# Performance work log

Hardware: AMD Instinct MI355X
Metric: run time of the kernel (lower is better)

Reference implementation:

```python
import jax, jax.numpy as jnp
import numpy as np

O, NI, F, D, NN, M = 2048, 16, 4, 128, 8, 8  # outfits, item slots, factors, dim, neighbors, valid slots
D2 = D // 2

def lrelu(x):
    return jax.nn.leaky_relu(x, 0.01)

def mlp2(x, W1, b1, W2, b2):
    # Linear -> LeakyReLU -> Linear -> LeakyReLU (Dropout is identity at inference)
    return lrelu(lrelu(x @ W1 + b1) @ W2 + b2)

def setup_inputs():
    ks = jax.random.split(jax.random.key(0), 16)
    s = 0.05
    pos = jnp.arange(NI)[None, :]
    outfit_items = jnp.where(pos < M, jax.random.randint(ks[0], (O, NI), 0, NI), -1)
    items_neighbor = jax.random.randint(ks[1], (O, NI, NN), -1, NI)
    items_feature = jax.random.normal(ks[2], (O, NI, D), dtype=jnp.float32)
    items_factors = jnp.zeros((O, NI, F, D), dtype=jnp.float32)
    p = {
        'cf_W1': jax.random.normal(ks[3], (F, D, D2)) * s,
        'cf_b1': jnp.zeros((F, D2)),
        'cf_W2': jax.random.normal(ks[4], (F, D2, D)) * s,
        'cf_b2': jnp.zeros((F, D)),
        'f2f_W1': jax.random.normal(ks[5], (D, D)) * s, 'f2f_b1': jnp.zeros((D,)),
        'f2f_W2': jax.random.normal(ks[6], (D, D)) * s, 'f2f_b2': jnp.zeros((D,)),
        'f2i_W1': jax.random.normal(ks[7], (D, D)) * s, 'f2i_b1': jnp.zeros((D,)),
        'f2i_W2': jax.random.normal(ks[8], (D, D)) * s, 'f2i_b2': jnp.zeros((D,)),
        'i2i_W1': jax.random.normal(ks[9], (D, D)) * s, 'i2i_b1': jnp.zeros((D,)),
        'i2i_W2': jax.random.normal(ks[10], (D, D)) * s, 'i2i_b2': jnp.zeros((D,)),
        'o2s_W': jax.random.normal(ks[11], (D, 1)) * s, 'o2s_b': jnp.zeros((1,)),
    }
    return dict(outfit_items=outfit_items, items_feature=items_feature,
                items_neighbor=items_neighbor, items_factors=items_factors, **p)

def _forward(outfit_items, items_feature, items_neighbor, items_factors,
             cf_W1, cf_b1, cf_W2, cf_b2, f2f_W1, f2f_b1, f2f_W2, f2f_b2,
             f2i_W1, f2i_b1, f2i_W2, f2i_b2, i2i_W1, i2i_b1, i2i_W2, i2i_b2,
             o2s_W, o2s_b):
    del items_factors  # creat_factors overwrites every entry in the original
    # --- creat_factors: per-factor 2-layer MLP on every item feature -> [O,NI,F,D]
    h = lrelu(jnp.einsum('oid,fde->oife', items_feature, cf_W1) + cf_b1)
    fac = lrelu(jnp.einsum('oife,fed->oifd', h, cf_W2) + cf_b2)

    # --- inter_factors: sequential over outfit slots; later slots read updated factors
    def outfit_fac(fac_o, oi_o, nbr_o):
        def step(f, i):
            valid = i != -1
            ic = jnp.maximum(i, 0)
            cand = jnp.concatenate([oi_o, nbr_o[ic]])                # [NI+NN]
            cm = (cand != -1) & (cand != i) & valid
            t = f[ic]                                                # [F,D] snapshot
            msg = mlp2(t[None] * f[jnp.maximum(cand, 0)],
                       f2f_W1, f2f_b1, f2f_W2, f2f_b2)               # [NI+NN,F,D]
            add = jnp.sum(jnp.where(cm[:, None, None], msg, 0.0), axis=0)
            return f.at[ic].add(jnp.where(valid, add, 0.0)), None
        f, _ = jax.lax.scan(step, fac_o, oi_o)
        return f
    fac = jax.vmap(outfit_fac)(fac, outfit_items, items_neighbor)

    # --- infer_items: feature[i] += sum_j f2i(fac[i,j]) for outfit members
    g = mlp2(fac, f2i_W1, f2i_b1, f2i_W2, f2i_b2).sum(axis=2)        # [O,NI,D]
    ic = jnp.maximum(outfit_items, 0)
    w = (outfit_items != -1).astype(g.dtype)                          # [O,NI]
    gsel = jnp.take_along_axis(g, ic[..., None], axis=1)
    scat = jax.vmap(lambda gs, idx, ww: jnp.zeros((NI, D), gs.dtype).at[idx].add(ww[:, None] * gs))
    feat = items_feature + scat(gsel, ic, w)

    # --- inter_items: sequential; current value detached (.data in original)
    def outfit_feat(fo_init, oi_o):
        jc = jnp.maximum(oi_o, 0)
        def step(fo, i):
            valid = i != -1
            ic_ = jnp.maximum(i, 0)
            t = jax.lax.stop_gradient(fo[ic_])
            msgs = mlp2(fo[jc], i2i_W1, i2i_b1, i2i_W2, i2i_b2)      # [NI,D]
            m = ((oi_o != -1) & (oi_o != i)).astype(fo.dtype)
            new = t + jnp.sum(m[:, None] * msgs, axis=0)
            return jnp.where(valid, fo.at[ic_].set(new), fo), None
        fo, _ = jax.lax.scan(step, fo_init, oi_o)
        return fo
    feat = jax.vmap(outfit_feat)(feat, outfit_items)

    # --- infer_outfit + score
    fsel = jnp.take_along_axis(feat, ic[..., None], axis=1)
    outfits = jnp.sum(w[..., None] * fsel, axis=1)                    # [O,D]
    scores = jax.nn.sigmoid(outfits @ o2s_W + o2s_b)[:, 0]            # [O]

    # --- com_loss: ||F F^T - I||_F^2 over valid slots (positional mask), / n_outfits
    G = jnp.einsum('oifd,oigd->oifg', fac, fac) - jnp.eye(F, dtype=fac.dtype)
    com = jnp.sum(w * jnp.sum(G * G, axis=(-1, -2))) / O
    return scores, jnp.reshape(com, (1,))

def reference(outfit_items, items_feature, items_neighbor, items_factors,
              cf_W1, cf_b1, cf_W2, cf_b2, f2f_W1, f2f_b1, f2f_W2, f2f_b2,
              f2i_W1, f2i_b1, f2i_W2, f2i_b2, i2i_W1, i2i_b1, i2i_W2, i2i_b2,
              o2s_W, o2s_b):
    return _forward(outfit_items, items_feature, items_neighbor, items_factors,
                    cf_W1, cf_b1, cf_W2, cf_b2, f2f_W1, f2f_b1, f2f_W2, f2f_b2,
                    f2i_W1, f2i_b1, f2i_W2, f2i_b2, i2i_W1, i2i_b1, i2i_W2, i2i_b2,
                    o2s_W, o2s_b)
```

## Files before the change

### kernel.cpp

```cpp
#include <hip/hip_runtime.h>
#include <hip/hip_bf16.h>
#include <math.h>


typedef __attribute__((ext_vector_type(8))) short short8;
typedef __attribute__((ext_vector_type(4))) float f32x4;

#define MFMA16(a, b, c) __builtin_amdgcn_mfma_f32_16x16x32_bf16(a, b, c, 0, 0, 0)

__device__ __forceinline__ float lrelu(float x) { return fmaxf(x, 0.01f * x); }

__device__ __forceinline__ ushort f2bf(float f) {
  unsigned u = __builtin_bit_cast(unsigned, f);
  u += 0x7fffu + ((u >> 16) & 1u);
  return (ushort)(u >> 16);
}
__device__ __forceinline__ float bflo(unsigned u) {
  return __builtin_bit_cast(float, u << 16);
}
__device__ __forceinline__ unsigned pk2(float a, float b) {
  float2 t; t.x = a; t.y = b;
  __hip_bfloat162 h = __float22bfloat162_rn(t);
  unsigned u;
  __builtin_memcpy(&u, &h, 4);
  return u;
}


__global__ __launch_bounds__(256) void prep_weights(
    const float* __restrict__ cfW1, const float* __restrict__ cfW2,
    const float* __restrict__ f2fW1, const float* __restrict__ f2fW2,
    const float* __restrict__ f2iW1, const float* __restrict__ f2iW2,
    const float* __restrict__ i2iW1, const float* __restrict__ i2iW2,
    ushort* __restrict__ ws, float* __restrict__ out) {
  const int idx = (int)(blockIdx.x * 256 + threadIdx.x);
  if (idx == 0) out[2048] = 0.0f;
  float v;
  if (idx < 32768) {
    int f = idx >> 13, r = idx & 8191, n = r >> 7, k = r & 127;
    v = cfW1[f * 8192 + k * 64 + n];
  } else if (idx < 65536) {
    int t = idx - 32768;
    int f = t >> 13, r = t & 8191, n = r >> 6, k = r & 63;
    v = cfW2[f * 8192 + k * 128 + n];
  } else {
    int t = idx - 65536;
    int seg = t >> 14, r = t & 16383, n = r >> 7, k = r & 127;
    const float* W = (seg == 0) ? f2fW1 : (seg == 1) ? f2fW2 :
                     (seg == 2) ? f2iW1 : (seg == 3) ? f2iW2 :
                     (seg == 4) ? i2iW1 : i2iW2;
    v = W[k * 128 + n];
  }
  ws[idx] = f2bf(v);
}

__global__ __launch_bounds__(512, 2) void mfgn_kernel(
    const int* __restrict__ outfit_items,
    const float* __restrict__ items_feature,
    const int* __restrict__ items_neighbor,
    const float* __restrict__ cfb1, const float* __restrict__ cfb2,
    const float* __restrict__ f2fb1, const float* __restrict__ f2fb2,
    const float* __restrict__ f2ib1, const float* __restrict__ f2ib2,
    const float* __restrict__ i2ib1, const float* __restrict__ i2ib2,
    const float* __restrict__ o2sW, const float* __restrict__ o2sb,
    const ushort* __restrict__ wsW,
    float* __restrict__ out)
{
  __shared__ float facL[16 * 528];
  __shared__ ushort prodS[8192] __attribute__((aligned(16)));
  __shared__ ushort hidS[8192] __attribute__((aligned(16)));
  __shared__ ushort featB[2048] __attribute__((aligned(16)));
  __shared__ float redE[8];
  __shared__ int oiL[16];
  __shared__ int clAll[256];
  __shared__ int ncAll[16];
  __shared__ int vslL[16];
  __shared__ int refcntL[16];
  __shared__ int nvsL;

  const int o = blockIdx.x;
  const int tid = (int)threadIdx.x;
  const int lane = tid & 63;
  const int wid = tid >> 6;
  const int n16 = lane & 15;
  const int q = lane >> 4;
  const int kb = q * 8;
  const int col = wid * 16 + n16;
  const int lx = lane * 8;
  const int fS = lane & 3, ciS = lane >> 2;
  const int kc0 = wid * 16;
  const int q0 = (wid & 1) * 2;
  const int sWA = ((wid >> 1) * 4 + (lane >> 4)) * 512 + (lane & 15) * 8;
  const int hwB = (wid >> 1) * 2048 + ((wid & 1) * 2 + (q >> 1)) * 128 + n16 * 8 + (q & 1) * 4;
  const int fbCol = (col >> 5) * 512 + ((col >> 3) & 3) * 128 + (col & 7);

  if (tid < 16) oiL[tid] = outfit_items[o * 16 + tid];
  {
    const int n = tid >> 5, d0 = (tid & 31) * 4;
    float4 v = *(const float4*)(items_feature + o * 2048 + tid * 4);
    uint2 pk; pk.x = pk2(v.x, v.y); pk.y = pk2(v.z, v.w);
    *(uint2*)(featB + (d0 >> 5) * 512 + (((d0 >> 3) & 3) * 16 + n) * 8 + (d0 & 7)) = pk;
  }
  if (tid == 0) {
    int cnt = 0;
    for (int s = 0; s < 16; ++s) refcntL[s] = 0;
    for (int s = 0; s < 16; ++s) {
      int v = oiL[s];
      if (v != -1) { vslL[cnt++] = s; refcntL[v]++; }
    }
    nvsL = cnt;
  }
  for (int s = wid; s < 16; s += 8) {
    const int iv = outfit_items[o * 16 + s];
    if (iv == -1) { if (lane == 0) ncAll[s] = 0; continue; }
    int cand = -1;
    if (lane < 24) cand = (lane < 16) ? outfit_items[o * 16 + lane]
                                      : items_neighbor[o * 128 + iv * 8 + (lane - 16)];
    bool ok = (lane < 24) && (cand != -1) && (cand != iv);
    unsigned long long bm = __ballot(ok);
    if (ok) clAll[s * 16 + __popcll(bm & ((1ull << lane) - 1ull))] = cand;
    if (lane == 0) ncAll[s] = (int)__popcll(bm);
  }
  __syncthreads();
  const int nvs = nvsL;

  {
    const int f = wid & 3, half = wid >> 2;
    short8 wA[2][4];
#pragma unroll
    for (int etl = 0; etl < 2; ++etl)
#pragma unroll
      for (int kt = 0; kt < 4; ++kt)
        wA[etl][kt] = *(const short8*)(wsW + (f * 64 + (half * 2 + etl) * 16 + n16) * 128
                                       + kt * 32 + kb);
    f32x4 acc[2];
#pragma unroll
    for (int etl = 0; etl < 2; ++etl)
      acc[etl] = *(const f32x4*)(cfb1 + f * 64 + (half * 2 + etl) * 16 + q * 4);
    for (int kt = 0; kt < 4; ++kt) {
      short8 x = *(const short8*)(featB + kt * 512 + lx);
      acc[0] = MFMA16(wA[0][kt], x, acc[0]);
      acc[1] = MFMA16(wA[1][kt], x, acc[1]);
    }
#pragma unroll
    for (int etl = 0; etl < 2; ++etl) {
      float h0 = lrelu(acc[etl][0]), h1 = lrelu(acc[etl][1]);
      float h2 = lrelu(acc[etl][2]), h3 = lrelu(acc[etl][3]);
      uint2 pk; pk.x = pk2(h0, h1); pk.y = pk2(h2, h3);
      *(uint2*)(hidS + half * 2048 + f * 512 + (etl * 2 + (q >> 1)) * 128
                + n16 * 8 + (q & 1) * 4) = pk;
    }
    __syncthreads();
    short8 wB[4][2];
#pragma unroll
    for (int ctl = 0; ctl < 4; ++ctl)
#pragma unroll
      for (int kt = 0; kt < 2; ++kt)
        wB[ctl][kt] = *(const short8*)(wsW + 32768 + (f * 128 + half * 64 + ctl * 16 + n16) * 64
                                       + kt * 32 + kb);
    f32x4 acc2[4];
#pragma unroll
    for (int ctl = 0; ctl < 4; ++ctl) {
      float b2 = cfb2[f * 128 + half * 64 + ctl * 16 + n16];
      acc2[ctl] = (f32x4){b2, b2, b2, b2};
    }
    for (int kt = 0; kt < 2; ++kt) {
      short8 h = *(const short8*)(hidS + (kt * 4 + f) * 512 + lx);
#pragma unroll
      for (int ctl = 0; ctl < 4; ++ctl) acc2[ctl] = MFMA16(h, wB[ctl][kt], acc2[ctl]);
    }
#pragma unroll
    for (int ctl = 0; ctl < 4; ++ctl) {
      int c = half * 64 + ctl * 16 + n16;
#pragma unroll
      for (int r = 0; r < 4; ++r)
        facL[(q * 4 + r) * 528 + f * 132 + c] = lrelu(acc2[ctl][r]);
    }
    __syncthreads();
  }

  {
    short8 w1f[4], w2f[4];
#pragma unroll
    for (int kt = 0; kt < 4; ++kt) {
      w1f[kt] = *(const short8*)(wsW + 65536 + col * 128 + kt * 32 + kb);
      w2f[kt] = *(const short8*)(wsW + 81920 + col * 128 + kt * 32 + kb);
    }
    const f32x4 b1q = *(const f32x4*)(f2fb1 + wid * 16 + q * 4);
    const float b2v = f2fb2[col];

    auto stageB = [&](int s, int iv_, int nc_) {
      if (ciS < nc_) {
        const int cit = clAll[s * 16 + ciS];
        const float* tp = facL + iv_ * 528 + fS * 132 + kc0;
        const float* cp = facL + cit * 528 + fS * 132 + kc0;
#pragma unroll
        for (int g = 0; g < 2; ++g) {
          float4 a0 = *(const float4*)(tp + g * 8), a1 = *(const float4*)(tp + g * 8 + 4);
          float4 c0 = *(const float4*)(cp + g * 8), c1 = *(const float4*)(cp + g * 8 + 4);
          uint4 u4;
          u4.x = pk2(a0.x * c0.x, a0.y * c0.y); u4.y = pk2(a0.z * c0.z, a0.w * c0.w);
          u4.z = pk2(a1.x * c1.x, a1.y * c1.y); u4.w = pk2(a1.z * c1.z, a1.w * c1.w);
          *(uint4*)(prodS + sWA + (q0 + g) * 128) = u4;
        }
      }
    };
    auto stageC = [&]() {
      const float* sp = facL + ciS * 528 + fS * 132 + kc0;
#pragma unroll
      for (int g = 0; g < 2; ++g) {
        float4 a0 = *(const float4*)(sp + g * 8), a1 = *(const float4*)(sp + g * 8 + 4);
        uint4 u4;
        u4.x = pk2(a0.x, a0.y); u4.y = pk2(a0.z, a0.w);
        u4.z = pk2(a1.x, a1.y); u4.w = pk2(a1.z, a1.w);
        *(uint4*)(prodS + sWA + (q0 + g) * 128) = u4;
      }
    };

    if (nvs > 0) { const int s0 = vslL[0]; stageB(s0, oiL[s0], ncAll[s0]); }
    __syncthreads();

    for (int u = 0; u < nvs; ++u) {
      const int s = vslL[u];
      const int iv = oiL[s];
      const int nc = ncAll[s];
      f32x4 acc[4];
#pragma unroll
      for (int mt = 0; mt < 4; ++mt) acc[mt] = b1q;
      for (int kt = 0; kt < 4; ++kt)
#pragma unroll
        for (int mt = 0; mt < 4; ++mt) {
          short8 x = *(const short8*)(prodS + (kt * 4 + mt) * 512 + lx);
          acc[mt] = MFMA16(w1f[kt], x, acc[mt]);
        }
#pragma unroll
      for (int mt = 0; mt < 4; ++mt) {
        float h0 = lrelu(acc[mt][0]), h1 = lrelu(acc[mt][1]);
        float h2 = lrelu(acc[mt][2]), h3 = lrelu(acc[mt][3]);
        uint2 pk; pk.x = pk2(h0, h1); pk.y = pk2(h2, h3);
        *(uint2*)(hidS + hwB + mt * 512) = pk;
      }
      __syncthreads();
      f32x4 acc2[4];
#pragma unroll
      for (int mt = 0; mt < 4; ++mt) acc2[mt] = (f32x4){b2v, b2v, b2v, b2v};
      for (int kt = 0; kt < 4; ++kt)
#pragma unroll
        for (int mt = 0; mt < 4; ++mt) {
          short8 h = *(const short8*)(hidS + (kt * 4 + mt) * 512 + lx);
          acc2[mt] = MFMA16(h, w2f[kt], acc2[mt]);
        }
      float part[4] = {0.f, 0.f, 0.f, 0.f};
#pragma unroll
      for (int mt = 0; mt < 4; ++mt) {
        bool act = (mt * 4 + q) < nc;
        if (act) {
#pragma unroll
          for (int r = 0; r < 4; ++r) part[r] += lrelu(acc2[mt][r]);
        }
      }
#pragma unroll
      for (int r = 0; r < 4; ++r) {
        float v = part[r];
        v += __shfl_xor(v, 16);
        v += __shfl_xor(v, 32);
        part[r] = v;
      }
      if (q == 0) {
#pragma unroll
        for (int r = 0; r < 4; ++r)
          facL[iv * 528 + r * 132 + col] += part[r];
      }
      if (u + 1 < nvs) {
        const int s2 = vslL[u + 1];
        stageB(s2, oiL[s2], ncAll[s2]);
      } else {
        stageC();
      }
      __syncthreads();
    }
    if (nvs == 0) { stageC(); __syncthreads(); }
  }

  {
    short8 w1f[4], w2f[4];
#pragma unroll
    for (int kt = 0; kt < 4; ++kt) {
      w1f[kt] = *(const short8*)(wsW + 98304 + col * 128 + kt * 32 + kb);
      w2f[kt] = *(const short8*)(wsW + 114688 + col * 128 + kt * 32 + kb);
    }
    const f32x4 b1q = *(const f32x4*)(f2ib1 + wid * 16 + q * 4);
    const float b2v = f2ib2[col];
    f32x4 acc[4];
#pragma unroll
    for (int mt = 0; mt < 4; ++mt) acc[mt] = b1q;
    for (int kt = 0; kt < 4; ++kt)
#pragma unroll
      for (int mt = 0; mt < 4; ++mt) {
        short8 x = *(const short8*)(prodS + (kt * 4 + mt) * 512 + lx);
        acc[mt] = MFMA16(w1f[kt], x, acc[mt]);
      }
#pragma unroll
    for (int mt = 0; mt < 4; ++mt) {
      float h0 = lrelu(acc[mt][0]), h1 = lrelu(acc[mt][1]);
      float h2 = lrelu(acc[mt][2]), h3 = lrelu(acc[mt][3]);
      uint2 pk; pk.x = pk2(h0, h1); pk.y = pk2(h2, h3);
      *(uint2*)(hidS + hwB + mt * 512) = pk;
    }
    __syncthreads();
    f32x4 acc2[4];
#pragma unroll
    for (int mt = 0; mt < 4; ++mt) acc2[mt] = (f32x4){b2v, b2v, b2v, b2v};
    for (int kt = 0; kt < 4; ++kt)
#pragma unroll
      for (int mt = 0; mt < 4; ++mt) {
        short8 h = *(const short8*)(hidS + (kt * 4 + mt) * 512 + lx);
        acc2[mt] = MFMA16(h, w2f[kt], acc2[mt]);
      }
#pragma unroll
    for (int mt = 0; mt < 4; ++mt) {
      int item = mt * 4 + q;
      float g = 0.f;
#pragma unroll
      for (int r = 0; r < 4; ++r) g += lrelu(acc2[mt][r]);
      int a = fbCol + item * 8;
      featB[a] = f2bf(bflo((unsigned)featB[a]) + (float)refcntL[item] * g);
    }
    __syncthreads();
  }

  {
    short8 w1f[4], w2f[4];
#pragma unroll
    for (int kt = 0; kt < 4; ++kt) {
      w1f[kt] = *(const short8*)(wsW + 131072 + col * 128 + kt * 32 + kb);
      w2f[kt] = *(const short8*)(wsW + 147456 + col * 128 + kt * 32 + kb);
    }
    const f32x4 b1q = *(const f32x4*)(i2ib1 + wid * 16 + q * 4);
    const float b2v = i2ib2[col];
    short8 xc[4];
#pragma unroll
    for (int kt = 0; kt < 4; ++kt)
      xc[kt] = *(const short8*)(featB + kt * 512 + lx);

    for (int u = 0; u < nvs; ++u) {
      const int iv = oiL[vslL[u]];
      f32x4 acc = b1q;
      for (int kt = 0; kt < 4; ++kt) acc = MFMA16(w1f[kt], xc[kt], acc);
      {
        float h0 = lrelu(acc[0]), h1 = lrelu(acc[1]);
        float h2 = lrelu(acc[2]), h3 = lrelu(acc[3]);
        uint2 pk; pk.x = pk2(h0, h1); pk.y = pk2(h2, h3);
        *(uint2*)(hidS + hwB) = pk;
      }
      __syncthreads();
      f32x4 acc2 = (f32x4){b2v, b2v, b2v, b2v};
      for (int kt = 0; kt < 4; ++kt) {
        short8 h = *(const short8*)(hidS + kt * 2048 + lx);
        acc2 = MFMA16(h, w2f[kt], acc2);
      }
      float part = 0.f;
#pragma unroll
      for (int r = 0; r < 4; ++r) {
        int item = q * 4 + r;
        float w = (item == iv) ? 0.0f : (float)refcntL[item];
        part += w * lrelu(acc2[r]);
      }
      part += __shfl_xor(part, 16);
      part += __shfl_xor(part, 32);
      if (q == 0) {
        int a = fbCol + iv * 8;
        featB[a] = f2bf(bflo((unsigned)featB[a]) + part);
      }
      __syncthreads();
      if (n16 == iv) {
#pragma unroll
        for (int kt = 0; kt < 4; ++kt)
          xc[kt] = *(const short8*)(featB + kt * 512 + lx);
      }
    }
  }

  if (tid < 128) {
    const int eb = (tid >> 5) * 512 + ((tid >> 3) & 3) * 128 + (tid & 7);
    float sum = 0.0f;
    for (int u = 0; u < nvs; ++u) {
      int it = oiL[vslL[u]];
      sum += bflo((unsigned)featB[eb + it * 8]);
    }
    float v = sum * o2sW[tid];
#pragma unroll
    for (int off = 1; off < 64; off <<= 1) v += __shfl_xor(v, off);
    if (lane == 0) redE[wid] = v;
  }
  __syncthreads();
  if (tid == 0) {
    float t = redE[0] + redE[1] + o2sb[0];
    out[o] = 1.0f / (1.0f + expf(-t));
  }

  {
    const int n = tid >> 5, f = (tid >> 3) & 3, g = (tid >> 1) & 3, h = tid & 1;
    float dot = 0.0f;
    if (f <= g) {
      const float* pa = facL + n * 528 + f * 132 + h * 64;
      const float* pb = facL + n * 528 + g * 132 + h * 64;
      for (int i = 0; i < 16; ++i) {
        float4 a = *(const float4*)(pa + i * 4);
        float4 b = *(const float4*)(pb + i * 4);
        dot += a.x * b.x + a.y * b.y + a.z * b.z + a.w * b.w;
      }
    }
    dot += __shfl_xor(dot, 1);
    float v = dot - ((f == g) ? 1.0f : 0.0f);
    float wgt = (f == g) ? 1.0f : 2.0f;
    float sq = (h == 0 && f <= g && oiL[n] != -1) ? wgt * v * v : 0.0f;
#pragma unroll
    for (int off = 1; off < 64; off <<= 1) sq += __shfl_xor(sq, off);
    __syncthreads();
    if (lane == 0) redE[wid] = sq;
    __syncthreads();
    if (tid == 0) {
      float tot = 0.f;
#pragma unroll
      for (int w = 0; w < 8; ++w) tot += redE[w];
      atomicAdd(out + 2048, tot * (1.0f / 2048.0f));
    }
  }
}

extern "C" void kernel_launch(void* const* d_in, const int* in_sizes, int n_in,
                              void* d_out, int out_size, void* d_ws, size_t ws_size,
                              hipStream_t stream) {
  float* out = (float*)d_out;
  ushort* ws = (ushort*)d_ws;
  hipLaunchKernelGGL(prep_weights, dim3(640), dim3(256), 0, stream,
                     (const float*)d_in[4], (const float*)d_in[6],
                     (const float*)d_in[8], (const float*)d_in[10],
                     (const float*)d_in[12], (const float*)d_in[14],
                     (const float*)d_in[16], (const float*)d_in[18],
                     ws, out);
  hipLaunchKernelGGL(mfgn_kernel, dim3(2048), dim3(512), 0, stream,
                     (const int*)d_in[0],
                     (const float*)d_in[1],
                     (const int*)d_in[2],
                     (const float*)d_in[5], (const float*)d_in[7],
                     (const float*)d_in[9], (const float*)d_in[11],
                     (const float*)d_in[13], (const float*)d_in[15],
                     (const float*)d_in[17], (const float*)d_in[19],
                     (const float*)d_in[20], (const float*)d_in[21],
                     (const ushort*)ws,
                     out);
}
```

Measured before the change: 320.9 us.

## Overlap next-slot staging with MLP and interleave Gram loss into i2i loop

In the f2f loop, the product staging for the next slot now runs right after the second MFMA stage instead of after the facL update. Rows that depend on the item just updated are recomputed afterwards, which moves most staging work off the critical path before the barrier. The com_loss Gram dot products are spread across the i2i loop barriers in small steps, and their reduction is merged into the final score write. This removes a separate tail phase and two barriers, but adds redundant staging work and a correctness risk if the dependency check misses a case.

```diff
diff --git a/kernel.cpp b/kernel.cpp
--- a/kernel.cpp
+++ b/kernel.cpp
@@ -71,6 +71,7 @@
   __shared__ ushort hidS[8192] __attribute__((aligned(16)));
   __shared__ ushort featB[2048] __attribute__((aligned(16)));
   __shared__ float redE[8];
+  __shared__ float redF[8];
   __shared__ int oiL[16];
   __shared__ int clAll[256];
   __shared__ int ncAll[16];
@@ -189,23 +190,20 @@
     const f32x4 b1q = *(const f32x4*)(f2fb1 + wid * 16 + q * 4);
     const float b2v = f2fb2[col];
 
-    auto stageB = [&](int s, int iv_, int nc_) {
-      if (ciS < nc_) {
-        const int cit = clAll[s * 16 + ciS];
-        const float* tp = facL + iv_ * 528 + fS * 132 + kc0;
-        const float* cp = facL + cit * 528 + fS * 132 + kc0;
-#pragma unroll
-        for (int g = 0; g < 2; ++g) {
-          float4 a0 = *(const float4*)(tp + g * 8), a1 = *(const float4*)(tp + g * 8 + 4);
-          float4 c0 = *(const float4*)(cp + g * 8), c1 = *(const float4*)(cp + g * 8 + 4);
-          uint4 u4;
-          u4.x = pk2(a0.x * c0.x, a0.y * c0.y); u4.y = pk2(a0.z * c0.z, a0.w * c0.w);
-          u4.z = pk2(a1.x * c1.x, a1.y * c1.y); u4.w = pk2(a1.z * c1.z, a1.w * c1.w);
-          *(uint4*)(prodS + sWA + (q0 + g) * 128) = u4;
-        }
+    auto stageRow = [&](int ivR, int citR) {
+      const float* tp = facL + ivR * 528 + fS * 132 + kc0;
+      const float* cp = facL + citR * 528 + fS * 132 + kc0;
+#pragma unroll
+      for (int g = 0; g < 2; ++g) {
+        float4 a0 = *(const float4*)(tp + g * 8), a1 = *(const float4*)(tp + g * 8 + 4);
+        float4 c0 = *(const float4*)(cp + g * 8), c1 = *(const float4*)(cp + g * 8 + 4);
+        uint4 u4;
+        u4.x = pk2(a0.x * c0.x, a0.y * c0.y); u4.y = pk2(a0.z * c0.z, a0.w * c0.w);
+        u4.z = pk2(a1.x * c1.x, a1.y * c1.y); u4.w = pk2(a1.z * c1.z, a1.w * c1.w);
+        *(uint4*)(prodS + sWA + (q0 + g) * 128) = u4;
       }
     };
-    auto stageC = [&]() {
+    auto stageCRow = [&]() {
       const float* sp = facL + ciS * 528 + fS * 132 + kc0;
 #pragma unroll
       for (int g = 0; g < 2; ++g) {
@@ -217,7 +215,10 @@
       }
     };
 
-    if (nvs > 0) { const int s0 = vslL[0]; stageB(s0, oiL[s0], ncAll[s0]); }
+    if (nvs > 0) {
+      const int s0 = vslL[0];
+      if (ciS < ncAll[s0]) stageRow(oiL[s0], clAll[s0 * 16 + ciS]);
+    }
     __syncthreads();
 
     for (int u = 0; u < nvs; ++u) {
@@ -250,6 +251,15 @@
           short8 h = *(const short8*)(hidS + (kt * 4 + mt) * 512 + lx);
           acc2[mt] = MFMA16(h, w2f[kt], acc2[mt]);
         }
+      const bool lastu = (u + 1 >= nvs);
+      int iv2 = -1, cit2 = -1;
+      if (!lastu) {
+        const int s2 = vslL[u + 1];
+        iv2 = oiL[s2];
+        if (ciS < ncAll[s2]) { cit2 = clAll[s2 * 16 + ciS]; stageRow(iv2, cit2); }
+      } else {
+        stageCRow();
+      }
       float part[4] = {0.f, 0.f, 0.f, 0.f};
 #pragma unroll
       for (int mt = 0; mt < 4; ++mt) {
@@ -271,15 +281,14 @@
         for (int r = 0; r < 4; ++r)
           facL[iv * 528 + r * 132 + col] += part[r];
       }
-      if (u + 1 < nvs) {
-        const int s2 = vslL[u + 1];
-        stageB(s2, oiL[s2], ncAll[s2]);
+      if (!lastu) {
+        if (cit2 >= 0 && (cit2 == iv || iv2 == iv)) stageRow(iv2, cit2);
       } else {
-        stageC();
+        if (ciS == iv) stageCRow();
       }
       __syncthreads();
     }
-    if (nvs == 0) { stageC(); __syncthreads(); }
+    if (nvs == 0) { stageCRow(); __syncthreads(); }
   }
 
   {
@@ -330,6 +339,20 @@
   }
 
   {
+    const int nF = tid >> 5, fF = (tid >> 3) & 3, gF = (tid >> 1) & 3, hF = tid & 1;
+    const float* paF = facL + nF * 528 + fF * 132 + hF * 64;
+    const float* pbF = facL + nF * 528 + gF * 132 + hF * 64;
+    float dotF = 0.0f;
+    int cF = (fF <= gF) ? 0 : 16;
+    auto fstep = [&]() {
+      if (cF < 16) {
+        float4 a = *(const float4*)(paF + cF * 4);
+        float4 b = *(const float4*)(pbF + cF * 4);
+        dotF += a.x * b.x + a.y * b.y + a.z * b.z + a.w * b.w;
+        ++cF;
+      }
+    };
+
     short8 w1f[4], w2f[4];
 #pragma unroll
     for (int kt = 0; kt < 4; ++kt) {
@@ -353,6 +376,7 @@
         uint2 pk; pk.x = pk2(h0, h1); pk.y = pk2(h2, h3);
         *(uint2*)(hidS + hwB) = pk;
       }
+      fstep();
       __syncthreads();
       f32x4 acc2 = (f32x4){b2v, b2v, b2v, b2v};
       for (int kt = 0; kt < 4; ++kt) {
@@ -372,6 +396,7 @@
         int a = fbCol + iv * 8;
         featB[a] = f2bf(bflo((unsigned)featB[a]) + part);
       }
+      fstep();
       __syncthreads();
       if (n16 == iv) {
 #pragma unroll
@@ -379,7 +404,17 @@
           xc[kt] = *(const short8*)(featB + kt * 512 + lx);
       }
     }
-  }
+
+    for (int t2 = 0; t2 < 16; ++t2) fstep();
+    dotF += __shfl_xor(dotF, 1);
+    float vF = dotF - ((fF == gF) ? 1.0f : 0.0f);
+    float wgtF = (fF == gF) ? 1.0f : 2.0f;
+    float sqF = (hF == 0 && fF <= gF && oiL[nF] != -1) ? wgtF * vF * vF : 0.0f;
+#pragma unroll
+    for (int off = 1; off < 64; off <<= 1) sqF += __shfl_xor(sqF, off);
+    if (lane == 0) redF[wid] = sqF;
+  }
+  __syncthreads();
 
   if (tid < 128) {
     const int eb = (tid >> 5) * 512 + ((tid >> 3) & 3) * 128 + (tid & 7);
@@ -397,35 +432,10 @@
   if (tid == 0) {
     float t = redE[0] + redE[1] + o2sb[0];
     out[o] = 1.0f / (1.0f + expf(-t));
-  }
-
-  {
-    const int n = tid >> 5, f = (tid >> 3) & 3, g = (tid >> 1) & 3, h = tid & 1;
-    float dot = 0.0f;
-    if (f <= g) {
-      const float* pa = facL + n * 528 + f * 132 + h * 64;
-      const float* pb = facL + n * 528 + g * 132 + h * 64;
-      for (int i = 0; i < 16; ++i) {
-        float4 a = *(const float4*)(pa + i * 4);
-        float4 b = *(const float4*)(pb + i * 4);
-        dot += a.x * b.x + a.y * b.y + a.z * b.z + a.w * b.w;
-      }
-    }
-    dot += __shfl_xor(dot, 1);
-    float v = dot - ((f == g) ? 1.0f : 0.0f);
-    float wgt = (f == g) ? 1.0f : 2.0f;
-    float sq = (h == 0 && f <= g && oiL[n] != -1) ? wgt * v * v : 0.0f;
-#pragma unroll
-    for (int off = 1; off < 64; off <<= 1) sq += __shfl_xor(sq, off);
-    __syncthreads();
-    if (lane == 0) redE[wid] = sq;
-    __syncthreads();
-    if (tid == 0) {
-      float tot = 0.f;
-#pragma unroll
-      for (int w = 0; w < 8; ++w) tot += redE[w];
-      atomicAdd(out + 2048, tot * (1.0f / 2048.0f));
-    }
+    float tot = 0.f;
+#pragma unroll
+    for (int w = 0; w < 8; ++w) tot += redF[w];
+    atomicAdd(out + 2048, tot * (1.0f / 2048.0f));
   }
 }
 
```

After: 325.7 us. About the same (+1.5%).

## Switch f2f and f2i MLPs to 32x32x16 MFMA tiles with 2D wave split

Applied to the files above, without the earlier changes.

Replaces the 16x16x32 MFMA formulation of the factor-to-factor and factor-to-item MLPs with 32x32x16 bf16 MFMAs. Waves are arranged as a 2x4 grid over rows and output columns, and the staging layout in shared memory is changed to match. Weights are now reloaded from global memory for each sequential slot step instead of being held in registers across the loop. Per-column reductions in f2f use shared-memory atomicAdd, and an extra barrier is added per iteration. The aim is fewer MFMA issues and less register pressure, at the cost of repeated weight loads, atomics and more synchronisation.

```diff
diff --git a/kernel.cpp b/kernel.cpp
--- a/kernel.cpp
+++ b/kernel.cpp
@@ -5,8 +5,10 @@
 
 typedef __attribute__((ext_vector_type(8))) short short8;
 typedef __attribute__((ext_vector_type(4))) float f32x4;
+typedef __attribute__((ext_vector_type(16))) float f32x16;
 
 #define MFMA16(a, b, c) __builtin_amdgcn_mfma_f32_16x16x32_bf16(a, b, c, 0, 0, 0)
+#define MFMA32(a, b, c) __builtin_amdgcn_mfma_f32_32x32x16_bf16(a, b, c, 0, 0, 0)
 
 __device__ __forceinline__ float lrelu(float x) { return fmaxf(x, 0.01f * x); }
 
@@ -87,10 +89,13 @@
   const int kb = q * 8;
   const int col = wid * 16 + n16;
   const int lx = lane * 8;
+  const int l31 = lane & 31;
+  const int h = lane >> 5;
+  const int rb = wid >> 2;
+  const int cb = wid & 3;
   const int fS = lane & 3, ciS = lane >> 2;
   const int kc0 = wid * 16;
-  const int q0 = (wid & 1) * 2;
-  const int sWA = ((wid >> 1) * 4 + (lane >> 4)) * 512 + (lane & 15) * 8;
+  const int ubase = (wid * 2 + h) * 512;
   const int hwB = (wid >> 1) * 2048 + ((wid & 1) * 2 + (q >> 1)) * 128 + n16 * 8 + (q & 1) * 4;
   const int fbCol = (col >> 5) * 512 + ((col >> 3) & 3) * 128 + (col & 7);
 
@@ -165,9 +170,9 @@
       acc2[ctl] = (f32x4){b2, b2, b2, b2};
     }
     for (int kt = 0; kt < 2; ++kt) {
-      short8 h = *(const short8*)(hidS + (kt * 4 + f) * 512 + lx);
-#pragma unroll
-      for (int ctl = 0; ctl < 4; ++ctl) acc2[ctl] = MFMA16(h, wB[ctl][kt], acc2[ctl]);
+      short8 hh = *(const short8*)(hidS + (kt * 4 + f) * 512 + lx);
+#pragma unroll
+      for (int ctl = 0; ctl < 4; ++ctl) acc2[ctl] = MFMA16(hh, wB[ctl][kt], acc2[ctl]);
     }
 #pragma unroll
     for (int ctl = 0; ctl < 4; ++ctl) {
@@ -180,14 +185,8 @@
   }
 
   {
-    short8 w1f[4], w2f[4];
-#pragma unroll
-    for (int kt = 0; kt < 4; ++kt) {
-      w1f[kt] = *(const short8*)(wsW + 65536 + col * 128 + kt * 32 + kb);
-      w2f[kt] = *(const short8*)(wsW + 81920 + col * 128 + kt * 32 + kb);
-    }
-    const f32x4 b1q = *(const f32x4*)(f2fb1 + wid * 16 + q * 4);
-    const float b2v = f2fb2[col];
+    const int wrow = cb * 32 + l31;
+    const int oc0 = cb * 32 + 4 * h;
 
     auto stageB = [&](int s, int iv_, int nc_) {
       if (ciS < nc_) {
@@ -201,11 +200,11 @@
           uint4 u4;
           u4.x = pk2(a0.x * c0.x, a0.y * c0.y); u4.y = pk2(a0.z * c0.z, a0.w * c0.w);
           u4.z = pk2(a1.x * c1.x, a1.y * c1.y); u4.w = pk2(a1.z * c1.z, a1.w * c1.w);
-          *(uint4*)(prodS + sWA + (q0 + g) * 128) = u4;
+          *(uint4*)(prodS + ubase + (l31 + g * 32) * 8) = u4;
         }
       }
     };
-    auto stageC = [&]() {
+    auto stageCRow = [&]() {
       const float* sp = facL + ciS * 528 + fS * 132 + kc0;
 #pragma unroll
       for (int g = 0; g < 2; ++g) {
@@ -213,7 +212,7 @@
         uint4 u4;
         u4.x = pk2(a0.x, a0.y); u4.y = pk2(a0.z, a0.w);
         u4.z = pk2(a1.x, a1.y); u4.w = pk2(a1.z, a1.w);
-        *(uint4*)(prodS + sWA + (q0 + g) * 128) = u4;
+        *(uint4*)(prodS + ubase + (l31 + g * 32) * 8) = u4;
       }
     };
 
@@ -224,107 +223,159 @@
       const int s = vslL[u];
       const int iv = oiL[s];
       const int nc = ncAll[s];
-      f32x4 acc[4];
-#pragma unroll
-      for (int mt = 0; mt < 4; ++mt) acc[mt] = b1q;
-      for (int kt = 0; kt < 4; ++kt)
-#pragma unroll
-        for (int mt = 0; mt < 4; ++mt) {
-          short8 x = *(const short8*)(prodS + (kt * 4 + mt) * 512 + lx);
-          acc[mt] = MFMA16(w1f[kt], x, acc[mt]);
-        }
-#pragma unroll
-      for (int mt = 0; mt < 4; ++mt) {
-        float h0 = lrelu(acc[mt][0]), h1 = lrelu(acc[mt][1]);
-        float h2 = lrelu(acc[mt][2]), h3 = lrelu(acc[mt][3]);
-        uint2 pk; pk.x = pk2(h0, h1); pk.y = pk2(h2, h3);
-        *(uint2*)(hidS + hwB + mt * 512) = pk;
+      {
+        short8 wf[8];
+#pragma unroll
+        for (int kt = 0; kt < 8; ++kt)
+          wf[kt] = *(const short8*)(wsW + 65536 + wrow * 128 + kt * 16 + h * 8);
+        float4 ba[4];
+#pragma unroll
+        for (int i = 0; i < 4; ++i)
+          ba[i] = *(const float4*)(f2fb1 + cb * 32 + i * 8 + h * 4);
+        f32x16 acc = {0.f,0.f,0.f,0.f, 0.f,0.f,0.f,0.f, 0.f,0.f,0.f,0.f, 0.f,0.f,0.f,0.f};
+        for (int kt = 0; kt < 8; ++kt) {
+          short8 x = *(const short8*)(prodS + (kt * 2 + rb) * 512 + lx);
+          acc = MFMA32(wf[kt], x, acc);
+        }
+#pragma unroll
+        for (int kt2 = 0; kt2 < 2; ++kt2)
+#pragma unroll
+          for (int hb = 0; hb < 2; ++hb) {
+            const int r0 = kt2 * 8 + hb * 4;
+            const float4 bb = ba[kt2 * 2 + hb];
+            float v0 = lrelu(acc[r0 + 0] + bb.x);
+            float v1 = lrelu(acc[r0 + 1] + bb.y);
+            float v2 = lrelu(acc[r0 + 2] + bb.z);
+            float v3 = lrelu(acc[r0 + 3] + bb.w);
+            uint2 pk; pk.x = pk2(v0, v1); pk.y = pk2(v2, v3);
+            *(uint2*)(hidS + ((cb * 2 + kt2) * 2 + rb) * 512 + (l31 | (hb << 5)) * 8 + h * 4) = pk;
+          }
       }
       __syncthreads();
-      f32x4 acc2[4];
-#pragma unroll
-      for (int mt = 0; mt < 4; ++mt) acc2[mt] = (f32x4){b2v, b2v, b2v, b2v};
-      for (int kt = 0; kt < 4; ++kt)
-#pragma unroll
-        for (int mt = 0; mt < 4; ++mt) {
-          short8 h = *(const short8*)(hidS + (kt * 4 + mt) * 512 + lx);
-          acc2[mt] = MFMA16(h, w2f[kt], acc2[mt]);
-        }
-      float part[4] = {0.f, 0.f, 0.f, 0.f};
-#pragma unroll
-      for (int mt = 0; mt < 4; ++mt) {
-        bool act = (mt * 4 + q) < nc;
-        if (act) {
-#pragma unroll
-          for (int r = 0; r < 4; ++r) part[r] += lrelu(acc2[mt][r]);
-        }
-      }
-#pragma unroll
-      for (int r = 0; r < 4; ++r) {
-        float v = part[r];
-        v += __shfl_xor(v, 16);
-        v += __shfl_xor(v, 32);
-        part[r] = v;
-      }
-      if (q == 0) {
-#pragma unroll
-        for (int r = 0; r < 4; ++r)
-          facL[iv * 528 + r * 132 + col] += part[r];
-      }
+      {
+        short8 wf[8];
+#pragma unroll
+        for (int kt = 0; kt < 8; ++kt)
+          wf[kt] = *(const short8*)(wsW + 81920 + wrow * 128 + kt * 16 + h * 8);
+        float4 ba[4];
+#pragma unroll
+        for (int i = 0; i < 4; ++i)
+          ba[i] = *(const float4*)(f2fb2 + cb * 32 + i * 8 + h * 4);
+        f32x16 acc2 = {0.f,0.f,0.f,0.f, 0.f,0.f,0.f,0.f, 0.f,0.f,0.f,0.f, 0.f,0.f,0.f,0.f};
+        for (int kt = 0; kt < 8; ++kt) {
+          short8 hh = *(const short8*)(hidS + (kt * 2 + rb) * 512 + lx);
+          acc2 = MFMA32(wf[kt], hh, acc2);
+        }
+        float b2r[16];
+#pragma unroll
+        for (int i = 0; i < 4; ++i) {
+          b2r[i * 4 + 0] = ba[i].x; b2r[i * 4 + 1] = ba[i].y;
+          b2r[i * 4 + 2] = ba[i].z; b2r[i * 4 + 3] = ba[i].w;
+        }
+        const bool act = (rb * 8 + (l31 >> 2)) < nc;
+        float part[16];
+#pragma unroll
+        for (int r = 0; r < 16; ++r) {
+          float v = lrelu(acc2[r] + b2r[r]);
+          part[r] = act ? v : 0.0f;
+        }
+#pragma unroll
+        for (int r = 0; r < 16; ++r) {
+          float v = part[r];
+          v += __shfl_xor(v, 4);
+          v += __shfl_xor(v, 8);
+          v += __shfl_xor(v, 16);
+          part[r] = v;
+        }
+        if (l31 < 4) {
+#pragma unroll
+          for (int r = 0; r < 16; ++r)
+            atomicAdd(&facL[iv * 528 + l31 * 132 + oc0 + (r & 3) + 8 * (r >> 2)], part[r]);
+        }
+      }
+      __syncthreads();
       if (u + 1 < nvs) {
         const int s2 = vslL[u + 1];
         stageB(s2, oiL[s2], ncAll[s2]);
       } else {
-        stageC();
+        stageCRow();
       }
       __syncthreads();
     }
-    if (nvs == 0) { stageC(); __syncthreads(); }
+    if (nvs == 0) { stageCRow(); __syncthreads(); }
   }
 
   {
-    short8 w1f[4], w2f[4];
-#pragma unroll
-    for (int kt = 0; kt < 4; ++kt) {
-      w1f[kt] = *(const short8*)(wsW + 98304 + col * 128 + kt * 32 + kb);
-      w2f[kt] = *(const short8*)(wsW + 114688 + col * 128 + kt * 32 + kb);
-    }
-    const f32x4 b1q = *(const f32x4*)(f2ib1 + wid * 16 + q * 4);
-    const float b2v = f2ib2[col];
-    f32x4 acc[4];
-#pragma unroll
-    for (int mt = 0; mt < 4; ++mt) acc[mt] = b1q;
-    for (int kt = 0; kt < 4; ++kt)
-#pragma unroll
-      for (int mt = 0; mt < 4; ++mt) {
-        short8 x = *(const short8*)(prodS + (kt * 4 + mt) * 512 + lx);
-        acc[mt] = MFMA16(w1f[kt], x, acc[mt]);
-      }
-#pragma unroll
-    for (int mt = 0; mt < 4; ++mt) {
-      float h0 = lrelu(acc[mt][0]), h1 = lrelu(acc[mt][1]);
-      float h2 = lrelu(acc[mt][2]), h3 = lrelu(acc[mt][3]);
-      uint2 pk; pk.x = pk2(h0, h1); pk.y = pk2(h2, h3);
-      *(uint2*)(hidS + hwB + mt * 512) = pk;
-    }
-    __syncthreads();
-    f32x4 acc2[4];
-#pragma unroll
-    for (int mt = 0; mt < 4; ++mt) acc2[mt] = (f32x4){b2v, b2v, b2v, b2v};
-    for (int kt = 0; kt < 4; ++kt)
-#pragma unroll
-      for (int mt = 0; mt < 4; ++mt) {
-        short8 h = *(const short8*)(hidS + (kt * 4 + mt) * 512 + lx);
-        acc2[mt] = MFMA16(h, w2f[kt], acc2[mt]);
-      }
-#pragma unroll
-    for (int mt = 0; mt < 4; ++mt) {
-      int item = mt * 4 + q;
-      float g = 0.f;
-#pragma unroll
-      for (int r = 0; r < 4; ++r) g += lrelu(acc2[mt][r]);
-      int a = fbCol + item * 8;
-      featB[a] = f2bf(bflo((unsigned)featB[a]) + (float)refcntL[item] * g);
+    const int wrow = cb * 32 + l31;
+    {
+      short8 wf[8];
+#pragma unroll
+      for (int kt = 0; kt < 8; ++kt)
+        wf[kt] = *(const short8*)(wsW + 98304 + wrow * 128 + kt * 16 + h * 8);
+      float4 ba[4];
+#pragma unroll
+      for (int i = 0; i < 4; ++i)
+        ba[i] = *(const float4*)(f2ib1 + cb * 32 + i * 8 + h * 4);
+      f32x16 acc = {0.f,0.f,0.f,0.f, 0.f,0.f,0.f,0.f, 0.f,0.f,0.f,0.f, 0.f,0.f,0.f,0.f};
+      for (int kt = 0; kt < 8; ++kt) {
+        short8 x = *(const short8*)(prodS + (kt * 2 + rb) * 512 + lx);
+        acc = MFMA32(wf[kt], x, acc);
+      }
+#pragma unroll
+      for (int kt2 = 0; kt2 < 2; ++kt2)
+#pragma unroll
+        for (int hb = 0; hb < 2; ++hb) {
+          const int r0 = kt2 * 8 + hb * 4;
+          const float4 bb = ba[kt2 * 2 + hb];
+          float v0 = lrelu(acc[r0 + 0] + bb.x);
+          float v1 = lrelu(acc[r0 + 1] + bb.y);
+          float v2 = lrelu(acc[r0 + 2] + bb.z);
+          float v3 = lrelu(acc[r0 + 3] + bb.w);
+          uint2 pk; pk.x = pk2(v0, v1); pk.y = pk2(v2, v3);
+          *(uint2*)(hidS + ((cb * 2 + kt2) * 2 + rb) * 512 + (l31 | (hb << 5)) * 8 + h * 4) = pk;
+        }
+    }
+    __syncthreads();
+    {
+      short8 wf[8];
+#pragma unroll
+      for (int kt = 0; kt < 8; ++kt)
+        wf[kt] = *(const short8*)(wsW + 114688 + wrow * 128 + kt * 16 + h * 8);
+      float4 ba[4];
+#pragma unroll
+      for (int i = 0; i < 4; ++i)
+        ba[i] = *(const float4*)(f2ib2 + cb * 32 + i * 8 + h * 4);
+      f32x16 acc2 = {0.f,0.f,0.f,0.f, 0.f,0.f,0.f,0.f, 0.f,0.f,0.f,0.f, 0.f,0.f,0.f,0.f};
+      for (int kt = 0; kt < 8; ++kt) {
+        short8 hh = *(const short8*)(hidS + (kt * 2 + rb) * 512 + lx);
+        acc2 = MFMA32(wf[kt], hh, acc2);
+      }
+      float b2r[16];
+#pragma unroll
+      for (int i = 0; i < 4; ++i) {
+        b2r[i * 4 + 0] = ba[i].x; b2r[i * 4 + 1] = ba[i].y;
+        b2r[i * 4 + 2] = ba[i].z; b2r[i * 4 + 3] = ba[i].w;
+      }
+      float gs[16];
+#pragma unroll
+      for (int r = 0; r < 16; ++r) gs[r] = lrelu(acc2[r] + b2r[r]);
+#pragma unroll
+      for (int r = 0; r < 16; ++r) {
+        float v = gs[r];
+        v += __shfl_xor(v, 1);
+        v += __shfl_xor(v, 2);
+        gs[r] = v;
+      }
+      if ((l31 & 3) == 0) {
+        const int item = rb * 8 + (l31 >> 2);
+        const float rc = (float)refcntL[item];
+#pragma unroll
+        for (int r = 0; r < 16; ++r) {
+          const int c = cb * 32 + (r & 3) + 8 * (r >> 2) + 4 * h;
+          const int a = (c >> 5) * 512 + (((c >> 3) & 3) * 16 + item) * 8 + (c & 7);
+          featB[a] = f2bf(bflo((unsigned)featB[a]) + rc * gs[r]);
+        }
+      }
     }
     __syncthreads();
   }
@@ -356,8 +407,8 @@
       __syncthreads();
       f32x4 acc2 = (f32x4){b2v, b2v, b2v, b2v};
       for (int kt = 0; kt < 4; ++kt) {
-        short8 h = *(const short8*)(hidS + kt * 2048 + lx);
-        acc2 = MFMA16(h, w2f[kt], acc2);
+        short8 hh = *(const short8*)(hidS + kt * 2048 + lx);
+        acc2 = MFMA16(hh, w2f[kt], acc2);
       }
       float part = 0.f;
 #pragma unroll
@@ -400,11 +451,11 @@
   }
 
   {
-    const int n = tid >> 5, f = (tid >> 3) & 3, g = (tid >> 1) & 3, h = tid & 1;
+    const int n = tid >> 5, f = (tid >> 3) & 3, g = (tid >> 1) & 3, hh = tid & 1;
     float dot = 0.0f;
     if (f <= g) {
-      const float* pa = facL + n * 528 + f * 132 + h * 64;
-      const float* pb = facL + n * 528 + g * 132 + h * 64;
+      const float* pa = facL + n * 528 + f * 132 + hh * 64;
+      const float* pb = facL + n * 528 + g * 132 + hh * 64;
       for (int i = 0; i < 16; ++i) {
         float4 a = *(const float4*)(pa + i * 4);
         float4 b = *(const float4*)(pb + i * 4);
@@ -414,7 +465,7 @@
     dot += __shfl_xor(dot, 1);
     float v = dot - ((f == g) ? 1.0f : 0.0f);
     float wgt = (f == g) ? 1.0f : 2.0f;
-    float sq = (h == 0 && f <= g && oiL[n] != -1) ? wgt * v * v : 0.0f;
+    float sq = (hh == 0 && f <= g && oiL[n] != -1) ? wgt * v * v : 0.0f;
 #pragma unroll
     for (int off = 1; off < 64; off <<= 1) sq += __shfl_xor(sq, off);
     __syncthreads();
```

New measurement: 572.9 us. +78.6%, slower.
